# Kernel optimization log

Measured on AMD Instinct MI355X. Metric: run time of the kernel, lower is better.

## Reference

```python
import jax, jax.numpy as jnp
import numpy as np

S = 32      # stochastic size
D = 600     # deterministic size
H = 600     # hidden size
A = 6       # action size
E = 1024    # encoder embed size
T = 50      # steps
B = 1024    # batch
MIN_STD = 0.1


def setup_inputs() -> dict:
    key = jax.random.key(0)
    ks = jax.random.split(key, 20)
    p = lambda k, shp: (jax.random.normal(k, shp, dtype=jnp.float32) * 0.02)
    inp = {
        "steps": T,
        "encoded": jax.random.normal(ks[0], (T, B, E), dtype=jnp.float32),
        "actions": jax.random.normal(ks[1], (T, B, A), dtype=jnp.float32),
        "init_stoch": jnp.zeros((B, S), dtype=jnp.float32),
        "init_det": jnp.zeros((B, D), dtype=jnp.float32),
        "noise_prior": jax.random.normal(ks[2], (T, B, S), dtype=jnp.float32),
        "noise_post": jax.random.normal(ks[3], (T, B, S), dtype=jnp.float32),
        # transition model: rnn input MLP
        "W_in": p(ks[4], (H, A + S)), "b_in": jnp.zeros((H,), jnp.float32),
        # GRUCell (torch layout: gates r,z,n)
        "W_ih": p(ks[5], (3 * D, H)), "W_hh": p(ks[6], (3 * D, D)),
        "b_ih": jnp.zeros((3 * D,), jnp.float32), "b_hh": jnp.zeros((3 * D,), jnp.float32),
        # stochastic prior model
        "Wp1": p(ks[7], (H, D)), "bp1": jnp.zeros((H,), jnp.float32),
        "Wp2": p(ks[8], (2 * S, H)), "bp2": jnp.zeros((2 * S,), jnp.float32),
        # stochastic posterior model
        "Wq1": p(ks[9], (H, D + E)), "bq1": jnp.zeros((H,), jnp.float32),
        "Wq2": p(ks[10], (2 * S, H)), "bq2": jnp.zeros((2 * S,), jnp.float32),
    }
    return inp


def _rollout(encoded, actions, init_stoch, init_det, noise_prior, noise_post,
             W_in, b_in, W_ih, W_hh, b_ih, b_hh, Wp1, bp1, Wp2, bp2, Wq1, bq1, Wq2, bq2):
    elu = jax.nn.elu

    def gru_cell(x, h):
        gi = x @ W_ih.T + b_ih          # [B, 3D]
        gh = h @ W_hh.T + b_hh          # [B, 3D]
        ir, iz, inn = jnp.split(gi, 3, axis=-1)
        hr, hz, hn = jnp.split(gh, 3, axis=-1)
        r = jax.nn.sigmoid(ir + hr)
        z = jax.nn.sigmoid(iz + hz)
        n = jnp.tanh(inn + r * hn)
        return (1.0 - z) * n + z * h

    def step(carry, inp):
        stoch, det = carry
        enc_t, act_t, eps_p, eps_q = inp
        # transition model (prior)
        rnn_in = elu(jnp.concatenate([act_t, stoch], axis=-1) @ W_in.T + b_in)
        det_new = gru_cell(rnn_in, det)
        pm, ps_raw = jnp.split(elu(det_new @ Wp1.T + bp1) @ Wp2.T + bp2, 2, axis=-1)
        ps = jax.nn.softplus(ps_raw) + MIN_STD
        prior_stoch = pm + ps * eps_p
        # representation model (posterior)
        y = jnp.concatenate([det_new, enc_t], axis=-1)
        qm, qs_raw = jnp.split(elu(y @ Wq1.T + bq1) @ Wq2.T + bq2, 2, axis=-1)
        qs = jax.nn.softplus(qs_raw) + MIN_STD
        post_stoch = qm + qs * eps_q
        outs = (pm, ps, prior_stoch, det_new, qm, qs, post_stoch, det_new)
        return (post_stoch, det_new), outs

    _, outs = jax.lax.scan(step, (init_stoch, init_det),
                           (encoded, actions, noise_prior, noise_post))
    return outs  # each [T, B, *]


def reference(steps, encoded, actions, init_stoch, init_det, noise_prior, noise_post,
              W_in, b_in, W_ih, W_hh, b_ih, b_hh, Wp1, bp1, Wp2, bp2, Wq1, bq1, Wq2, bq2):
    # steps == T; scan rolls out the full horizon.
    return _rollout(encoded[:steps], actions[:steps], init_stoch, init_det,
                    noise_prior[:steps], noise_post[:steps],
                    W_in, b_in, W_ih, W_hh, b_ih, b_hh,
                    Wp1, bp1, Wp2, bp2, Wq1, bq1, Wq2, bq2)
```

## Files before the change

### kernel.cpp

```cpp
#include <hip/hip_runtime.h>

#define MFMA16 __builtin_amdgcn_mfma_f32_16x16x32_bf16

typedef __attribute__((ext_vector_type(8))) short short8;
typedef __attribute__((ext_vector_type(4))) float floatx4;

static constexpr int T_STEPS = 50;
static constexpr int BATCH   = 1024;
static constexpr int SDIM    = 32;
static constexpr int DDIM    = 600;
static constexpr int ADIM    = 6;
static constexpr int KP      = 608;
static constexpr int PITCH   = 616;
static constexpr int SAPITCH = 72;
static constexpr int NWAVES  = 10;
static constexpr int NTHREADS = 640;

static constexpr size_t SZ608    = (size_t)608 * 608;
static constexpr size_t OFF_WIHR = 0;
static constexpr size_t OFF_WIHZ = OFF_WIHR + SZ608;
static constexpr size_t OFF_WIHN = OFF_WIHZ + SZ608;
static constexpr size_t OFF_WHHR = OFF_WIHN + SZ608;
static constexpr size_t OFF_WHHZ = OFF_WHHR + SZ608;
static constexpr size_t OFF_WHHN = OFF_WHHZ + SZ608;
static constexpr size_t OFF_WP1  = OFF_WHHN + SZ608;
static constexpr size_t OFF_WQ1D = OFF_WP1  + SZ608;
static constexpr size_t OFF_WQ1E = OFF_WQ1D + SZ608;
static constexpr size_t OFF_WSA  = OFF_WQ1E + (size_t)608 * 1024;
static constexpr size_t OFF_WHEAD= OFF_WSA  + (size_t)608 * 64;
static constexpr size_t OFF_PREQ = OFF_WHEAD+ (size_t)128 * 608;
static constexpr size_t OFF_DETG = OFF_PREQ + (size_t)T_STEPS * BATCH * 600;
static constexpr size_t OFF_BAR  = OFF_DETG + (size_t)BATCH * KP;
static constexpr size_t OFF_PART = OFF_BAR + 256;

static constexpr size_t O_PM = 0;
static constexpr size_t O_PS = 1638400;
static constexpr size_t O_PR = 3276800;
static constexpr size_t O_D1 = 4915200;
static constexpr size_t O_QM = 35635200;
static constexpr size_t O_QS = 37273600;
static constexpr size_t O_PO = 38912000;
static constexpr size_t O_D2 = 40550400;

__device__ __forceinline__ unsigned short f2bf(float f) {
  unsigned u = __float_as_uint(f);
  u += 0x7FFFu + ((u >> 16) & 1u);
  return (unsigned short)(u >> 16);
}
__device__ __forceinline__ float bf2f(unsigned short u) {
  return __uint_as_float(((unsigned)u) << 16);
}
__device__ __forceinline__ float elu_f(float v) { return v > 0.f ? v : expm1f(v); }
__device__ __forceinline__ float sigmoid_f(float x) { return 1.f / (1.f + expf(-x)); }
__device__ __forceinline__ float tanh_f(float x) {
  x = fminf(fmaxf(x, -15.f), 15.f);
  float e = expf(2.f * x);
  return (e - 1.f) / (e + 1.f);
}

__global__ __launch_bounds__(256) void stage_weights(
    const float* __restrict__ Win, const float* __restrict__ Wih, const float* __restrict__ Whh,
    const float* __restrict__ Wp1, const float* __restrict__ Wq1,
    const float* __restrict__ Wp2, const float* __restrict__ Wq2,
    unsigned short* __restrict__ ws)
{
  const int region = blockIdx.y;
  if (region == 11) {
    if (blockIdx.x == 0 && threadIdx.x < 64)
      ((int*)(ws + OFF_BAR))[threadIdx.x] = 0;
    return;
  }
  int R = 608, C = 608;
  size_t dst = 0;
  switch (region) {
    case 0: dst = OFF_WIHR; break;
    case 1: dst = OFF_WIHZ; break;
    case 2: dst = OFF_WIHN; break;
    case 3: dst = OFF_WHHR; break;
    case 4: dst = OFF_WHHZ; break;
    case 5: dst = OFF_WHHN; break;
    case 6: dst = OFF_WP1;  break;
    case 7: dst = OFF_WQ1D; break;
    case 8: dst = OFF_WQ1E; C = 1024; break;
    case 9: dst = OFF_WSA;  C = 64;   break;
    case 10: dst = OFF_WHEAD; R = 128; break;
  }
  const int total = R * C;
  for (int e = blockIdx.x * 256 + threadIdx.x; e < total; e += gridDim.x * 256) {
    int n = e / C, k = e - n * C;
    float v = 0.f;
    switch (region) {
      case 0: if (n < 600 && k < 600) v = Wih[(size_t)n * 600 + k]; break;
      case 1: if (n < 600 && k < 600) v = Wih[(size_t)(600 + n) * 600 + k]; break;
      case 2: if (n < 600 && k < 600) v = Wih[(size_t)(1200 + n) * 600 + k]; break;
      case 3: if (n < 600 && k < 600) v = Whh[(size_t)n * 600 + k]; break;
      case 4: if (n < 600 && k < 600) v = Whh[(size_t)(600 + n) * 600 + k]; break;
      case 5: if (n < 600 && k < 600) v = Whh[(size_t)(1200 + n) * 600 + k]; break;
      case 6: if (n < 600 && k < 600) v = Wp1[(size_t)n * 600 + k]; break;
      case 7: if (n < 600 && k < 600) v = Wq1[(size_t)n * 1624 + k]; break;
      case 8: if (n < 600) v = Wq1[(size_t)n * 1624 + 600 + k]; break;
      case 9: if (n < 600) { if (k < 32) v = Win[(size_t)n * 38 + 6 + k];
                             else if (k < 38) v = Win[(size_t)n * 38 + (k - 32)]; } break;
      case 10: if (k < 600) v = (n < 64) ? Wp2[(size_t)n * 600 + k]
                                         : Wq2[(size_t)(n - 64) * 600 + k]; break;
    }
    ws[dst + (size_t)e] = f2bf(v);
  }
}

__global__ __launch_bounds__(256) void preq_gemm(
    const float* __restrict__ enc, const float* __restrict__ bq1,
    const unsigned short* __restrict__ ws, unsigned short* __restrict__ preq)
{
  __shared__ unsigned short A[16 * 1032];
  const size_t g0 = (size_t)blockIdx.x * 16;
  const int tid = threadIdx.x;

  const float4* e4 = (const float4*)(enc + g0 * 1024);
  for (int i = tid; i < 16 * 256; i += 256) {
    int row = i >> 8, c4 = i & 255;
    float4 v = e4[row * 256 + c4];
    int base = row * 1032 + c4 * 4;
    A[base + 0] = f2bf(v.x); A[base + 1] = f2bf(v.y);
    A[base + 2] = f2bf(v.z); A[base + 3] = f2bf(v.w);
  }
  __syncthreads();

  const int wave = tid >> 6, lane = tid & 63, q = lane >> 4, l15 = lane & 15;
  const unsigned short* Wq1e = ws + OFF_WQ1E;
  for (int tile = wave; tile < 38; tile += 4) {
    const int n0 = tile * 16;
    floatx4 acc = {0.f, 0.f, 0.f, 0.f};
    const unsigned short* wb = Wq1e + (size_t)(n0 + l15) * 1024 + q * 8;
    const int aoff = l15 * 1032 + q * 8;
    for (int ki = 0; ki < 32; ++ki) {
      short8 a = *(const short8*)(&A[aoff + ki * 32]);
      short8 b = *(const short8*)(wb + ki * 32);
      acc = MFMA16(a, b, acc, 0, 0, 0);
    }
    const int col = n0 + l15;
    if (col < 600) {
      float bb = bq1[col];
      for (int i = 0; i < 4; ++i) {
        int row = q * 4 + i;
        preq[(g0 + row) * 600 + col] = f2bf(acc[i] + bb);
      }
    }
  }
}

__global__ __launch_bounds__(NTHREADS)
__attribute__((amdgpu_waves_per_eu(3)))
void rssm_rollout(
    const float* __restrict__ actions, const float* __restrict__ init_stoch,
    const float* __restrict__ init_det,
    const float* __restrict__ eps_p, const float* __restrict__ eps_q,
    const float* __restrict__ b_in, const float* __restrict__ b_ih, const float* __restrict__ b_hh,
    const float* __restrict__ bp1, const float* __restrict__ bp2, const float* __restrict__ bq2,
    unsigned short* __restrict__ wsm, float* __restrict__ out)
{
  __shared__ unsigned short XB[16 * PITCH];
  __shared__ unsigned short DC[16 * PITCH];
  __shared__ unsigned short HQ[16 * PITCH];
  __shared__ unsigned short SA[16 * SAPITCH];

  const unsigned short* ws = wsm;
  const int tid  = threadIdx.x;
  const int wave = tid >> 6, lane = tid & 63, q = lane >> 4, l15 = lane & 15;
  const int wg    = blockIdx.x;
  const int slice = wg & 3;
  const int bg    = wg >> 2;
  const int brow0 = bg * 16;
  const int ntile = (slice < 3) ? 10 : 8;
  const int tile0 = slice * 10;
  const int cs    = slice * 160;

  unsigned short* DETG = wsm + OFF_DETG;
  int*   bar  = (int*)(wsm + OFF_BAR);
  float* PART = (float*)(wsm + OFF_PART);
  const unsigned short* preq = ws + OFF_PREQ;

  float* out_pm = out + O_PM; float* out_ps = out + O_PS; float* out_pr = out + O_PR;
  float* out_d1 = out + O_D1; float* out_qm = out + O_QM; float* out_qs = out + O_QS;
  float* out_po = out + O_PO; float* out_d2 = out + O_D2;

  int phase = 0;
  auto bgsync = [&]() {
    __syncthreads();
    ++phase;
    if (tid == 0) {
      __hip_atomic_fetch_add(&bar[bg], 1, __ATOMIC_RELAXED, __HIP_MEMORY_SCOPE_AGENT);
      while (__hip_atomic_load(&bar[bg], __ATOMIC_RELAXED, __HIP_MEMORY_SCOPE_AGENT) < 4 * phase)
        __builtin_amdgcn_s_sleep(2);
    }
    __syncthreads();
    asm volatile("" ::: "memory");
  };

  auto do_reduce = [&](int tcur) {
    const volatile float* part = (const volatile float*)(PART + (size_t)bg * (4 * 16 * 128));
    if (tid < 512) {
      const int r = tid >> 5, c = tid & 31;
      float pm = bp2[c], psr = bp2[32 + c];
      float qm = bq2[c], qsr = bq2[32 + c];
      for (int s2 = 0; s2 < 4; ++s2) {
        const volatile float* p = part + (s2 * 16 + r) * 128;
        pm += p[c];       psr += p[32 + c];
        qm += p[64 + c];  qsr += p[96 + c];
      }
      const size_t oidx = ((size_t)(tcur - 1) * BATCH + brow0 + r) * SDIM + c;
      const float qs = (qsr > 30.f ? qsr : log1pf(expf(qsr))) + 0.1f;
      const float x  = qm + qs * eps_q[oidx];
      SA[r * SAPITCH + c] = f2bf(x);
      if (slice == 0) {
        const float ps = (psr > 30.f ? psr : log1pf(expf(psr))) + 0.1f;
        out_pm[oidx] = pm; out_ps[oidx] = ps; out_pr[oidx] = pm + ps * eps_p[oidx];
      } else if (slice == 1) {
        out_qm[oidx] = qm; out_qs[oidx] = qs; out_po[oidx] = x;
      }
    }
  };

  for (int t = 0; t < T_STEPS; ++t) {
    if (t == 0) {
      for (int i = tid; i < 16 * PITCH; i += NTHREADS) { XB[i] = 0; DC[i] = 0; HQ[i] = 0; }
      for (int i = tid; i < 16 * SAPITCH; i += NTHREADS) SA[i] = 0;
      __syncthreads();
      for (int i = tid; i < 16 * SDIM; i += NTHREADS) {
        int r = i >> 5, c = i & 31;
        SA[r * SAPITCH + c] = f2bf(init_stoch[(size_t)(brow0 + r) * SDIM + c]);
      }
      for (int i = tid; i < 16 * DDIM; i += NTHREADS) {
        int r = i / DDIM, k = i - r * DDIM;
        DC[r * PITCH + k] = f2bf(init_det[(size_t)(brow0 + r) * DDIM + k]);
      }
      if (tid < 128) {
        int r = tid >> 3, c = 600 + (tid & 7);
        *(volatile unsigned short*)&DETG[(size_t)(brow0 + r) * KP + c] = 0;
      }
    } else {
      do_reduce(t);
    }
    if (tid < 96) {
      int r = tid / 6, j = tid - r * 6;
      SA[r * SAPITCH + 32 + j] = f2bf(actions[((size_t)t * BATCH + brow0 + r) * ADIM + j]);
    }
    __syncthreads();

    for (int tile = wave; tile < 38; tile += NWAVES) {
      const int n0 = tile * 16;
      floatx4 acc = {0.f, 0.f, 0.f, 0.f};
      const unsigned short* wb = ws + OFF_WSA + (size_t)(n0 + l15) * 64 + q * 8;
      const int aoff = l15 * SAPITCH + q * 8;
      acc = MFMA16(*(const short8*)(&SA[aoff]),      *(const short8*)(wb),      acc, 0, 0, 0);
      acc = MFMA16(*(const short8*)(&SA[aoff + 32]), *(const short8*)(wb + 32), acc, 0, 0, 0);
      const int col = n0 + l15;
      if (col < DDIM) {
        float bi = b_in[col];
        for (int i = 0; i < 4; ++i)
          XB[(q * 4 + i) * PITCH + col] = f2bf(elu_f(acc[i] + bi));
      }
    }
    __syncthreads();

    if (wave < ntile) {
      const int n0 = (tile0 + wave) * 16;
      floatx4 aIr = {0,0,0,0}, aIz = {0,0,0,0}, aIn = {0,0,0,0};
      floatx4 aHr = {0,0,0,0}, aHz = {0,0,0,0}, aHn = {0,0,0,0};
      const size_t wrow = (size_t)(n0 + l15) * KP + q * 8;
      const unsigned short* pIr = ws + OFF_WIHR + wrow;
      const unsigned short* pIz = ws + OFF_WIHZ + wrow;
      const unsigned short* pIn = ws + OFF_WIHN + wrow;
      const unsigned short* pHr = ws + OFF_WHHR + wrow;
      const unsigned short* pHz = ws + OFF_WHHZ + wrow;
      const unsigned short* pHn = ws + OFF_WHHN + wrow;
      const int aoff = l15 * PITCH + q * 8;
      #pragma unroll 4
      for (int ki = 0; ki < 19; ++ki) {
        short8 ax = *(const short8*)(&XB[aoff + ki * 32]);
        short8 ad = *(const short8*)(&DC[aoff + ki * 32]);
        aIr = MFMA16(ax, *(const short8*)(pIr + ki * 32), aIr, 0, 0, 0);
        aIz = MFMA16(ax, *(const short8*)(pIz + ki * 32), aIz, 0, 0, 0);
        aIn = MFMA16(ax, *(const short8*)(pIn + ki * 32), aIn, 0, 0, 0);
        aHr = MFMA16(ad, *(const short8*)(pHr + ki * 32), aHr, 0, 0, 0);
        aHz = MFMA16(ad, *(const short8*)(pHz + ki * 32), aHz, 0, 0, 0);
        aHn = MFMA16(ad, *(const short8*)(pHn + ki * 32), aHn, 0, 0, 0);
      }
      const int d = n0 + l15;
      if (d < DDIM) {
        float bihr = b_ih[d],        bhhr = b_hh[d];
        float bihz = b_ih[600 + d],  bhhz = b_hh[600 + d];
        float bihn = b_ih[1200 + d], bhhn = b_hh[1200 + d];
        for (int i = 0; i < 4; ++i) {
          int row = q * 4 + i;
          float r = sigmoid_f(aIr[i] + aHr[i] + bihr + bhhr);
          float z = sigmoid_f(aIz[i] + aHz[i] + bihz + bhhz);
          float n = tanh_f(aIn[i] + bihn + r * (aHn[i] + bhhn));
          float dprev = bf2f(DC[row * PITCH + d]);
          float dn = (1.f - z) * n + z * dprev;
          *(volatile unsigned short*)&DETG[(size_t)(brow0 + row) * KP + d] = f2bf(dn);
          size_t oidx = ((size_t)t * BATCH + brow0 + row) * DDIM + d;
          out_d1[oidx] = dn;
          out_d2[oidx] = dn;
        }
      }
    }
    bgsync();

    {
      const volatile unsigned long long* src =
          (const volatile unsigned long long*)DETG;
      for (int i = tid; i < 16 * 152; i += NTHREADS) {
        int r = i / 152, c = i - r * 152;
        *(unsigned long long*)(&DC[r * PITCH + c * 4]) = src[(size_t)(brow0 + r) * 152 + c];
      }
    }
    __syncthreads();

    if (wave < ntile) {
      const int n0 = (tile0 + wave) * 16;
      floatx4 accP = {0,0,0,0}, accQ = {0,0,0,0};
      const size_t wrow = (size_t)(n0 + l15) * KP + q * 8;
      const unsigned short* pP = ws + OFF_WP1  + wrow;
      const unsigned short* pQ = ws + OFF_WQ1D + wrow;
      const int aoff = l15 * PITCH + q * 8;
      #pragma unroll 4
      for (int ki = 0; ki < 19; ++ki) {
        short8 a = *(const short8*)(&DC[aoff + ki * 32]);
        accP = MFMA16(a, *(const short8*)(pP + ki * 32), accP, 0, 0, 0);
        accQ = MFMA16(a, *(const short8*)(pQ + ki * 32), accQ, 0, 0, 0);
      }
      const int col = n0 + l15;
      if (col < DDIM) {
        float bb = bp1[col];
        for (int i = 0; i < 4; ++i) {
          int row = q * 4 + i;
          XB[row * PITCH + col] = f2bf(elu_f(accP[i] + bb));
          float pre = bf2f(preq[((size_t)t * BATCH + brow0 + row) * 600 + col]);
          HQ[row * PITCH + col] = f2bf(elu_f(accQ[i] + pre));
        }
      }
    }
    __syncthreads();

    if (wave < 8) {
      const int h0 = wave * 16;
      const unsigned short* Asrc = (wave < 4) ? XB : HQ;
      const int nk = (slice < 3) ? 5 : 4;
      floatx4 acc = {0,0,0,0};
      const unsigned short* pW = ws + OFF_WHEAD + (size_t)(h0 + l15) * KP + cs + q * 8;
      const int abase = l15 * PITCH + cs + q * 8;
      for (int kk = 0; kk < nk; ++kk) {
        acc = MFMA16(*(const short8*)(&Asrc[abase + kk * 32]),
                     *(const short8*)(pW + kk * 32), acc, 0, 0, 0);
      }
      volatile float* pdst = (volatile float*)(PART + (size_t)(bg * 4 + slice) * (16 * 128));
      for (int i = 0; i < 4; ++i)
        pdst[(q * 4 + i) * 128 + h0 + l15] = acc[i];
    }
    bgsync();
  }

  do_reduce(T_STEPS);
}

extern "C" void kernel_launch(void* const* d_in, const int* in_sizes, int n_in,
                              void* d_out, int out_size, void* d_ws, size_t ws_size,
                              hipStream_t stream) {
  const float* enc    = (const float*)d_in[1];
  const float* act    = (const float*)d_in[2];
  const float* init_s = (const float*)d_in[3];
  const float* init_d = (const float*)d_in[4];
  const float* np_    = (const float*)d_in[5];
  const float* nq_    = (const float*)d_in[6];
  const float* Win    = (const float*)d_in[7];
  const float* b_in   = (const float*)d_in[8];
  const float* Wih    = (const float*)d_in[9];
  const float* Whh    = (const float*)d_in[10];
  const float* bih    = (const float*)d_in[11];
  const float* bhh    = (const float*)d_in[12];
  const float* Wp1    = (const float*)d_in[13];
  const float* bp1    = (const float*)d_in[14];
  const float* Wp2    = (const float*)d_in[15];
  const float* bp2    = (const float*)d_in[16];
  const float* Wq1    = (const float*)d_in[17];
  const float* bq1    = (const float*)d_in[18];
  const float* Wq2    = (const float*)d_in[19];
  const float* bq2    = (const float*)d_in[20];
  unsigned short* ws  = (unsigned short*)d_ws;
  float* out = (float*)d_out;

  stage_weights<<<dim3(256, 12), 256, 0, stream>>>(Win, Wih, Whh, Wp1, Wq1, Wp2, Wq2, ws);
  preq_gemm<<<3200, 256, 0, stream>>>(enc, bq1, ws, ws + OFF_PREQ);
  rssm_rollout<<<256, NTHREADS, 0, stream>>>(act, init_s, init_d, np_, nq_,
                                             b_in, bih, bhh, bp1, bp2, bq2, ws, out);
}
```

Baseline: 4.025 ms.

## Software-prefetch weight fragments, batch loads, use nontemporal stores, relax waves_per_eu

```diff
diff --git a/kernel.cpp b/kernel.cpp
--- a/kernel.cpp
+++ b/kernel.cpp
@@ -150,7 +150,7 @@
 }
 
 __global__ __launch_bounds__(NTHREADS)
-__attribute__((amdgpu_waves_per_eu(3)))
+__attribute__((amdgpu_waves_per_eu(2)))
 void rssm_rollout(
     const float* __restrict__ actions, const float* __restrict__ init_stoch,
     const float* __restrict__ init_det,
@@ -201,22 +201,31 @@
     const volatile float* part = (const volatile float*)(PART + (size_t)bg * (4 * 16 * 128));
     if (tid < 512) {
       const int r = tid >> 5, c = tid & 31;
-      float pm = bp2[c], psr = bp2[32 + c];
-      float qm = bq2[c], qsr = bq2[32 + c];
-      for (int s2 = 0; s2 < 4; ++s2) {
-        const volatile float* p = part + (s2 * 16 + r) * 128;
-        pm += p[c];       psr += p[32 + c];
-        qm += p[64 + c];  qsr += p[96 + c];
-      }
+      const volatile float* p0 = part + (0 * 16 + r) * 128;
+      const volatile float* p1 = part + (1 * 16 + r) * 128;
+      const volatile float* p2 = part + (2 * 16 + r) * 128;
+      const volatile float* p3 = part + (3 * 16 + r) * 128;
+      float a00 = p0[c], a01 = p0[32 + c], a02 = p0[64 + c], a03 = p0[96 + c];
+      float a10 = p1[c], a11 = p1[32 + c], a12 = p1[64 + c], a13 = p1[96 + c];
+      float a20 = p2[c], a21 = p2[32 + c], a22 = p2[64 + c], a23 = p2[96 + c];
+      float a30 = p3[c], a31 = p3[32 + c], a32 = p3[64 + c], a33 = p3[96 + c];
+      float pm  = bp2[c]      + a00 + a10 + a20 + a30;
+      float psr = bp2[32 + c] + a01 + a11 + a21 + a31;
+      float qm  = bq2[c]      + a02 + a12 + a22 + a32;
+      float qsr = bq2[32 + c] + a03 + a13 + a23 + a33;
       const size_t oidx = ((size_t)(tcur - 1) * BATCH + brow0 + r) * SDIM + c;
       const float qs = (qsr > 30.f ? qsr : log1pf(expf(qsr))) + 0.1f;
       const float x  = qm + qs * eps_q[oidx];
       SA[r * SAPITCH + c] = f2bf(x);
       if (slice == 0) {
         const float ps = (psr > 30.f ? psr : log1pf(expf(psr))) + 0.1f;
-        out_pm[oidx] = pm; out_ps[oidx] = ps; out_pr[oidx] = pm + ps * eps_p[oidx];
+        __builtin_nontemporal_store(pm, &out_pm[oidx]);
+        __builtin_nontemporal_store(ps, &out_ps[oidx]);
+        __builtin_nontemporal_store(pm + ps * eps_p[oidx], &out_pr[oidx]);
       } else if (slice == 1) {
-        out_qm[oidx] = qm; out_qs[oidx] = qs; out_po[oidx] = x;
+        __builtin_nontemporal_store(qm, &out_qm[oidx]);
+        __builtin_nontemporal_store(qs, &out_qs[oidx]);
+        __builtin_nontemporal_store(x,  &out_po[oidx]);
       }
     }
   };
@@ -252,8 +261,12 @@
       floatx4 acc = {0.f, 0.f, 0.f, 0.f};
       const unsigned short* wb = ws + OFF_WSA + (size_t)(n0 + l15) * 64 + q * 8;
       const int aoff = l15 * SAPITCH + q * 8;
-      acc = MFMA16(*(const short8*)(&SA[aoff]),      *(const short8*)(wb),      acc, 0, 0, 0);
-      acc = MFMA16(*(const short8*)(&SA[aoff + 32]), *(const short8*)(wb + 32), acc, 0, 0, 0);
+      short8 a0 = *(const short8*)(&SA[aoff]);
+      short8 a1 = *(const short8*)(&SA[aoff + 32]);
+      short8 b0 = *(const short8*)(wb);
+      short8 b1 = *(const short8*)(wb + 32);
+      acc = MFMA16(a0, b0, acc, 0, 0, 0);
+      acc = MFMA16(a1, b1, acc, 0, 0, 0);
       const int col = n0 + l15;
       if (col < DDIM) {
         float bi = b_in[col];
@@ -275,16 +288,27 @@
       const unsigned short* pHz = ws + OFF_WHHZ + wrow;
       const unsigned short* pHn = ws + OFF_WHHN + wrow;
       const int aoff = l15 * PITCH + q * 8;
-      #pragma unroll 4
+      short8 cIr, cIz, cIn, cHr, cHz, cHn;
+      short8 nIr, nIz, nIn, nHr, nHz, nHn;
+      cIr = *(const short8*)(pIr); cIz = *(const short8*)(pIz); cIn = *(const short8*)(pIn);
+      cHr = *(const short8*)(pHr); cHz = *(const short8*)(pHz); cHn = *(const short8*)(pHn);
+      #pragma unroll
       for (int ki = 0; ki < 19; ++ki) {
+        if (ki < 18) {
+          const int o = (ki + 1) * 32;
+          nIr = *(const short8*)(pIr + o); nIz = *(const short8*)(pIz + o);
+          nIn = *(const short8*)(pIn + o); nHr = *(const short8*)(pHr + o);
+          nHz = *(const short8*)(pHz + o); nHn = *(const short8*)(pHn + o);
+        }
         short8 ax = *(const short8*)(&XB[aoff + ki * 32]);
         short8 ad = *(const short8*)(&DC[aoff + ki * 32]);
-        aIr = MFMA16(ax, *(const short8*)(pIr + ki * 32), aIr, 0, 0, 0);
-        aIz = MFMA16(ax, *(const short8*)(pIz + ki * 32), aIz, 0, 0, 0);
-        aIn = MFMA16(ax, *(const short8*)(pIn + ki * 32), aIn, 0, 0, 0);
-        aHr = MFMA16(ad, *(const short8*)(pHr + ki * 32), aHr, 0, 0, 0);
-        aHz = MFMA16(ad, *(const short8*)(pHz + ki * 32), aHz, 0, 0, 0);
-        aHn = MFMA16(ad, *(const short8*)(pHn + ki * 32), aHn, 0, 0, 0);
+        aIr = MFMA16(ax, cIr, aIr, 0, 0, 0);
+        aIz = MFMA16(ax, cIz, aIz, 0, 0, 0);
+        aIn = MFMA16(ax, cIn, aIn, 0, 0, 0);
+        aHr = MFMA16(ad, cHr, aHr, 0, 0, 0);
+        aHz = MFMA16(ad, cHz, aHz, 0, 0, 0);
+        aHn = MFMA16(ad, cHn, aHn, 0, 0, 0);
+        cIr = nIr; cIz = nIz; cIn = nIn; cHr = nHr; cHz = nHz; cHn = nHn;
       }
       const int d = n0 + l15;
       if (d < DDIM) {
@@ -300,8 +324,8 @@
           float dn = (1.f - z) * n + z * dprev;
           *(volatile unsigned short*)&DETG[(size_t)(brow0 + row) * KP + d] = f2bf(dn);
           size_t oidx = ((size_t)t * BATCH + brow0 + row) * DDIM + d;
-          out_d1[oidx] = dn;
-          out_d2[oidx] = dn;
+          __builtin_nontemporal_store(dn, &out_d1[oidx]);
+          __builtin_nontemporal_store(dn, &out_d2[oidx]);
         }
       }
     }
@@ -310,10 +334,20 @@
     {
       const volatile unsigned long long* src =
           (const volatile unsigned long long*)DETG;
-      for (int i = tid; i < 16 * 152; i += NTHREADS) {
-        int r = i / 152, c = i - r * 152;
-        *(unsigned long long*)(&DC[r * PITCH + c * 4]) = src[(size_t)(brow0 + r) * 152 + c];
-      }
+      const int i0 = tid, i1 = tid + 640, i2 = tid + 1280, i3 = tid + 1920;
+      const int r0 = i0 / 152, c0 = i0 - r0 * 152;
+      const int r1 = i1 / 152, c1 = i1 - r1 * 152;
+      const int r2 = i2 / 152, c2 = i2 - r2 * 152;
+      const int r3 = i3 / 152, c3 = i3 - r3 * 152;
+      unsigned long long v0, v1, v2, v3 = 0;
+      v0 = src[(size_t)(brow0 + r0) * 152 + c0];
+      v1 = src[(size_t)(brow0 + r1) * 152 + c1];
+      v2 = src[(size_t)(brow0 + r2) * 152 + c2];
+      if (i3 < 2432) v3 = src[(size_t)(brow0 + r3) * 152 + c3];
+      *(unsigned long long*)(&DC[r0 * PITCH + c0 * 4]) = v0;
+      *(unsigned long long*)(&DC[r1 * PITCH + c1 * 4]) = v1;
+      *(unsigned long long*)(&DC[r2 * PITCH + c2 * 4]) = v2;
+      if (i3 < 2432) *(unsigned long long*)(&DC[r3 * PITCH + c3 * 4]) = v3;
     }
     __syncthreads();
 
@@ -324,11 +358,19 @@
       const unsigned short* pP = ws + OFF_WP1  + wrow;
       const unsigned short* pQ = ws + OFF_WQ1D + wrow;
       const int aoff = l15 * PITCH + q * 8;
-      #pragma unroll 4
+      short8 b0P, b0Q, b1P, b1Q, b2P, b2Q;
+      b0P = *(const short8*)(pP);      b0Q = *(const short8*)(pQ);
+      b1P = *(const short8*)(pP + 32); b1Q = *(const short8*)(pQ + 32);
+      #pragma unroll
       for (int ki = 0; ki < 19; ++ki) {
+        if (ki < 17) {
+          const int o = (ki + 2) * 32;
+          b2P = *(const short8*)(pP + o); b2Q = *(const short8*)(pQ + o);
+        }
         short8 a = *(const short8*)(&DC[aoff + ki * 32]);
-        accP = MFMA16(a, *(const short8*)(pP + ki * 32), accP, 0, 0, 0);
-        accQ = MFMA16(a, *(const short8*)(pQ + ki * 32), accQ, 0, 0, 0);
+        accP = MFMA16(a, b0P, accP, 0, 0, 0);
+        accQ = MFMA16(a, b0Q, accQ, 0, 0, 0);
+        b0P = b1P; b0Q = b1Q; b1P = b2P; b1Q = b2Q;
       }
       const int col = n0 + l15;
       if (col < DDIM) {
@@ -336,7 +378,8 @@
         for (int i = 0; i < 4; ++i) {
           int row = q * 4 + i;
           XB[row * PITCH + col] = f2bf(elu_f(accP[i] + bb));
-          float pre = bf2f(preq[((size_t)t * BATCH + brow0 + row) * 600 + col]);
+          float pre = bf2f(__builtin_nontemporal_load(
+              &preq[((size_t)t * BATCH + brow0 + row) * 600 + col]));
           HQ[row * PITCH + col] = f2bf(elu_f(accQ[i] + pre));
         }
       }
@@ -346,14 +389,24 @@
     if (wave < 8) {
       const int h0 = wave * 16;
       const unsigned short* Asrc = (wave < 4) ? XB : HQ;
-      const int nk = (slice < 3) ? 5 : 4;
       floatx4 acc = {0,0,0,0};
       const unsigned short* pW = ws + OFF_WHEAD + (size_t)(h0 + l15) * KP + cs + q * 8;
       const int abase = l15 * PITCH + cs + q * 8;
-      for (int kk = 0; kk < nk; ++kk) {
-        acc = MFMA16(*(const short8*)(&Asrc[abase + kk * 32]),
-                     *(const short8*)(pW + kk * 32), acc, 0, 0, 0);
-      }
+      short8 w0, w1, w2, w3, w4 = {};
+      short8 a0, a1, a2, a3, a4 = {};
+      w0 = *(const short8*)(pW);       w1 = *(const short8*)(pW + 32);
+      w2 = *(const short8*)(pW + 64);  w3 = *(const short8*)(pW + 96);
+      a0 = *(const short8*)(&Asrc[abase]);      a1 = *(const short8*)(&Asrc[abase + 32]);
+      a2 = *(const short8*)(&Asrc[abase + 64]); a3 = *(const short8*)(&Asrc[abase + 96]);
+      if (slice < 3) {
+        w4 = *(const short8*)(pW + 128);
+        a4 = *(const short8*)(&Asrc[abase + 128]);
+      }
+      acc = MFMA16(a0, w0, acc, 0, 0, 0);
+      acc = MFMA16(a1, w1, acc, 0, 0, 0);
+      acc = MFMA16(a2, w2, acc, 0, 0, 0);
+      acc = MFMA16(a3, w3, acc, 0, 0, 0);
+      if (slice < 3) acc = MFMA16(a4, w4, acc, 0, 0, 0);
       volatile float* pdst = (volatile float*)(PART + (size_t)(bg * 4 + slice) * (16 * 128));
       for (int i = 0; i < 4; ++i)
         pdst[(q * 4 + i) * 128 + h0 + l15] = acc[i];
```

Measured after the change: 3.618 ms. -10.1%, faster.
